# Kernel tuning notes

Measured on AMD Instinct MI355X. Metric: run time of the kernel, lower is better.

Reference implementation:

```python
import jax, jax.numpy as jnp
import numpy as np

GAMMA = 1.0

def setup_inputs() -> dict:
    key = jax.random.key(0)
    kx, ky = jax.random.split(key)
    X = jax.random.normal(kx, (8192, 64), dtype=jnp.float32)
    Y = jax.random.normal(ky, (8192, 64), dtype=jnp.float32)
    return {"X": X, "Y": Y}

def reference(X, Y):
    x2 = jnp.sum(X * X, axis=-1)            # (n,)
    y2 = jnp.sum(Y * Y, axis=-1)            # (m,)
    xy = X @ Y.T                            # (n, m)
    dist2 = x2[:, None] + y2[None, :] - 2.0 * xy
    dist2 = jnp.maximum(dist2, 0.0)         # numerical guard
    return jnp.exp(-GAMMA * dist2)
```

## Files before the change

kernel.cpp:

```cpp
#include <hip/hip_runtime.h>

typedef __attribute__((ext_vector_type(8))) short  short8_t;
typedef __attribute__((ext_vector_type(8))) unsigned short ushort8_t;
typedef __attribute__((ext_vector_type(4))) float  floatx4;

constexpr int N_ROWS = 8192;
constexpr int DIM    = 64;
constexpr int TILE   = 128;

__device__ __forceinline__ unsigned short bf16_rne(float f) {
    unsigned int u = __float_as_uint(f);
    u += 0x7FFFu + ((u >> 16) & 1u);
    return (unsigned short)(u >> 16);
}

__global__ void __launch_bounds__(256)
row_norms_kernel(const float* __restrict__ X, const float* __restrict__ Y,
                 float* __restrict__ x2, float* __restrict__ y2) {
    const int r = blockIdx.x * blockDim.x + threadIdx.x;
    const float4* xr = reinterpret_cast<const float4*>(X + (size_t)r * DIM);
    const float4* yr = reinterpret_cast<const float4*>(Y + (size_t)r * DIM);
    float sx = 0.f, sy = 0.f;
#pragma unroll
    for (int j = 0; j < DIM / 4; ++j) {
        float4 a = xr[j];
        sx = fmaf(a.x, a.x, fmaf(a.y, a.y, fmaf(a.z, a.z, fmaf(a.w, a.w, sx))));
        float4 b = yr[j];
        sy = fmaf(b.x, b.x, fmaf(b.y, b.y, fmaf(b.z, b.z, fmaf(b.w, b.w, sy))));
    }
    x2[r] = sx;
    y2[r] = sy;
}

__global__ void __launch_bounds__(256, 2)
rbf_mfma_kernel(const float* __restrict__ X, const float* __restrict__ Y,
                const float* __restrict__ x2, const float* __restrict__ y2,
                float* __restrict__ out) {
    __shared__ unsigned short smem[4 * TILE * DIM];
    constexpr int XH = 0 * TILE * DIM;
    constexpr int XL = 1 * TILE * DIM;
    constexpr int YH = 2 * TILE * DIM;
    constexpr int YL = 3 * TILE * DIM;

    const int tid  = threadIdx.x;
    const int row0 = blockIdx.y * TILE;
    const int col0 = blockIdx.x * TILE;

    {
        const int r = tid >> 1;
        const int h = tid & 1;
        const float* xr = X + (size_t)(row0 + r) * DIM + h * 32;
        const float* yr = Y + (size_t)(col0 + r) * DIM + h * 32;
        const int swz = (r & 7) * 8;
#pragma unroll
        for (int jj = 0; jj < 4; ++jj) {
            const int k0  = h * 32 + jj * 8;
            const int idx = ((r * DIM + k0) ^ swz);
            float f[8];
            *reinterpret_cast<float4*>(&f[0]) = *reinterpret_cast<const float4*>(xr + jj * 8);
            *reinterpret_cast<float4*>(&f[4]) = *reinterpret_cast<const float4*>(xr + jj * 8 + 4);
            ushort8_t hi, lo;
#pragma unroll
            for (int e = 0; e < 8; ++e) {
                unsigned short hh = bf16_rne(f[e]);
                hi[e] = hh;
                lo[e] = bf16_rne(f[e] - __uint_as_float((unsigned int)hh << 16));
            }
            *reinterpret_cast<ushort8_t*>(&smem[XH + idx]) = hi;
            *reinterpret_cast<ushort8_t*>(&smem[XL + idx]) = lo;

            *reinterpret_cast<float4*>(&f[0]) = *reinterpret_cast<const float4*>(yr + jj * 8);
            *reinterpret_cast<float4*>(&f[4]) = *reinterpret_cast<const float4*>(yr + jj * 8 + 4);
#pragma unroll
            for (int e = 0; e < 8; ++e) {
                unsigned short hh = bf16_rne(f[e]);
                hi[e] = hh;
                lo[e] = bf16_rne(f[e] - __uint_as_float((unsigned int)hh << 16));
            }
            *reinterpret_cast<ushort8_t*>(&smem[YH + idx]) = hi;
            *reinterpret_cast<ushort8_t*>(&smem[YL + idx]) = lo;
        }
    }
    __syncthreads();

    const int lane = tid & 63;
    const int w    = tid >> 6;
    const int wr   = (w >> 1) * 64;
    const int wc   = (w & 1) * 64;
    const int li   = lane & 15;
    const int lg   = lane >> 4;

    floatx4 acc[4][4] = {};

    const int kfrag = lg * 8;
#define FRAG(base, rowbase, ks)                                                \
    (*reinterpret_cast<const short8_t*>(                                       \
        &smem[(base) + ((((rowbase) + li) * DIM + (ks) * 32 + kfrag)           \
                        ^ ((((rowbase) + li) & 7) * 8))]))

    const int stepA[6] = {XH, XH, XH, XH, XL, XL};
    const int stepB[6] = {YH, YH, YL, YL, YH, YH};
    const int stepK[6] = {0, 1, 0, 1, 0, 1};
#pragma unroll
    for (int s = 0; s < 6; ++s) {
        short8_t a[4], b[4];
#pragma unroll
        for (int mi = 0; mi < 4; ++mi) a[mi] = FRAG(stepA[s], wr + mi * 16, stepK[s]);
#pragma unroll
        for (int ni = 0; ni < 4; ++ni) b[ni] = FRAG(stepB[s], wc + ni * 16, stepK[s]);
#pragma unroll
        for (int mi = 0; mi < 4; ++mi)
#pragma unroll
            for (int ni = 0; ni < 4; ++ni)
                acc[mi][ni] = __builtin_amdgcn_mfma_f32_16x16x32_bf16(
                    a[mi], b[ni], acc[mi][ni], 0, 0, 0);
    }
#undef FRAG

    float ys[4];
#pragma unroll
    for (int ni = 0; ni < 4; ++ni) ys[ni] = y2[col0 + wc + ni * 16 + li];

#pragma unroll
    for (int mi = 0; mi < 4; ++mi) {
        const int rbase = row0 + wr + mi * 16 + lg * 4;
#pragma unroll
        for (int j = 0; j < 4; ++j) {
            const float xs = x2[rbase + j];
            float* orow = out + (size_t)(rbase + j) * N_ROWS + col0 + wc + li;
#pragma unroll
            for (int ni = 0; ni < 4; ++ni) {
                float d = fmaf(-2.f, acc[mi][ni][j], xs + ys[ni]);
                d = fmaxf(d, 0.f);
                orow[ni * 16] = __expf(-d);
            }
        }
    }
}

extern "C" void kernel_launch(void* const* d_in, const int* in_sizes, int n_in,
                              void* d_out, int out_size, void* d_ws, size_t ws_size,
                              hipStream_t stream) {
    const float* X = (const float*)d_in[0];
    const float* Y = (const float*)d_in[1];
    float* out = (float*)d_out;
    float* x2  = (float*)d_ws;
    float* y2  = x2 + N_ROWS;

    row_norms_kernel<<<N_ROWS / 256, 256, 0, stream>>>(X, Y, x2, y2);

    dim3 grid(N_ROWS / TILE, N_ROWS / TILE);
    rbf_mfma_kernel<<<grid, 256, 0, stream>>>(X, Y, x2, y2, out);
}
```

Baseline: 72.68 us.

## Precompute bf16 hi/lo split panels once and DMA them into LDS

```diff
diff --git a/kernel.cpp b/kernel.cpp
--- a/kernel.cpp
+++ b/kernel.cpp
@@ -1,12 +1,13 @@
 #include <hip/hip_runtime.h>
 
-typedef __attribute__((ext_vector_type(8))) short  short8_t;
+typedef __attribute__((ext_vector_type(8))) short          short8_t;
 typedef __attribute__((ext_vector_type(8))) unsigned short ushort8_t;
-typedef __attribute__((ext_vector_type(4))) float  floatx4;
+typedef __attribute__((ext_vector_type(4))) float          floatx4;
 
 constexpr int N_ROWS = 8192;
 constexpr int DIM    = 64;
 constexpr int TILE   = 128;
+constexpr int PANEL  = TILE * DIM;
 
 __device__ __forceinline__ unsigned short bf16_rne(float f) {
     unsigned int u = __float_as_uint(f);
@@ -14,126 +15,143 @@
     return (unsigned short)(u >> 16);
 }
 
+typedef __attribute__((address_space(1))) unsigned int gu32;
+typedef __attribute__((address_space(3))) unsigned int lu32;
+__device__ __forceinline__ void gload16(const void* g, void* l) {
+    __builtin_amdgcn_global_load_lds((gu32*)g, (lu32*)l, 16, 0, 0);
+}
+
 __global__ void __launch_bounds__(256)
-row_norms_kernel(const float* __restrict__ X, const float* __restrict__ Y,
-                 float* __restrict__ x2, float* __restrict__ y2) {
-    const int r = blockIdx.x * blockDim.x + threadIdx.x;
+split_norms_kernel(const float* __restrict__ X, const float* __restrict__ Y,
+                   float* __restrict__ x2, float* __restrict__ y2,
+                   unsigned short* __restrict__ Xs, unsigned short* __restrict__ Ys) {
+    const int r  = blockIdx.x * 256 + threadIdx.x;
+    const int p  = r >> 7;
+    const int rl = r & 127;
+    const int swz = (rl & 7) * 8;
+    const size_t pb = (size_t)p * (2 * PANEL);
+
     const float4* xr = reinterpret_cast<const float4*>(X + (size_t)r * DIM);
     const float4* yr = reinterpret_cast<const float4*>(Y + (size_t)r * DIM);
+
     float sx = 0.f, sy = 0.f;
 #pragma unroll
-    for (int j = 0; j < DIM / 4; ++j) {
-        float4 a = xr[j];
-        sx = fmaf(a.x, a.x, fmaf(a.y, a.y, fmaf(a.z, a.z, fmaf(a.w, a.w, sx))));
-        float4 b = yr[j];
-        sy = fmaf(b.x, b.x, fmaf(b.y, b.y, fmaf(b.z, b.z, fmaf(b.w, b.w, sy))));
+    for (int c = 0; c < 8; ++c) {
+        const int off = (rl * DIM + c * 8) ^ swz;
+        float f[8];
+        ushort8_t hi, lo;
+
+        *reinterpret_cast<float4*>(&f[0]) = xr[2 * c];
+        *reinterpret_cast<float4*>(&f[4]) = xr[2 * c + 1];
+#pragma unroll
+        for (int e = 0; e < 8; ++e) {
+            sx = fmaf(f[e], f[e], sx);
+            unsigned short hh = bf16_rne(f[e]);
+            hi[e] = hh;
+            lo[e] = bf16_rne(f[e] - __uint_as_float((unsigned int)hh << 16));
+        }
+        *reinterpret_cast<ushort8_t*>(&Xs[pb + off])         = hi;
+        *reinterpret_cast<ushort8_t*>(&Xs[pb + PANEL + off]) = lo;
+
+        *reinterpret_cast<float4*>(&f[0]) = yr[2 * c];
+        *reinterpret_cast<float4*>(&f[4]) = yr[2 * c + 1];
+#pragma unroll
+        for (int e = 0; e < 8; ++e) {
+            sy = fmaf(f[e], f[e], sy);
+            unsigned short hh = bf16_rne(f[e]);
+            hi[e] = hh;
+            lo[e] = bf16_rne(f[e] - __uint_as_float((unsigned int)hh << 16));
+        }
+        *reinterpret_cast<ushort8_t*>(&Ys[pb + off])         = hi;
+        *reinterpret_cast<ushort8_t*>(&Ys[pb + PANEL + off]) = lo;
     }
     x2[r] = sx;
     y2[r] = sy;
 }
 
 __global__ void __launch_bounds__(256, 2)
-rbf_mfma_kernel(const float* __restrict__ X, const float* __restrict__ Y,
+rbf_mfma_kernel(const unsigned short* __restrict__ Xs,
+                const unsigned short* __restrict__ Ys,
                 const float* __restrict__ x2, const float* __restrict__ y2,
                 float* __restrict__ out) {
-    __shared__ unsigned short smem[4 * TILE * DIM];
-    constexpr int XH = 0 * TILE * DIM;
-    constexpr int XL = 1 * TILE * DIM;
-    constexpr int YH = 2 * TILE * DIM;
-    constexpr int YL = 3 * TILE * DIM;
+    __shared__ unsigned short smem[4 * PANEL];
 
     const int tid  = threadIdx.x;
+    const int lane = tid & 63;
+    const int w    = tid >> 6;
     const int row0 = blockIdx.y * TILE;
     const int col0 = blockIdx.x * TILE;
 
     {
-        const int r = tid >> 1;
-        const int h = tid & 1;
-        const float* xr = X + (size_t)(row0 + r) * DIM + h * 32;
-        const float* yr = Y + (size_t)(col0 + r) * DIM + h * 32;
-        const int swz = (r & 7) * 8;
+        const unsigned short* src =
+            (w < 2) ? Xs + (size_t)blockIdx.y * (2 * PANEL) + w * PANEL
+                    : Ys + (size_t)blockIdx.x * (2 * PANEL) + (w & 1) * PANEL;
+        unsigned short* dst = &smem[w * PANEL];
 #pragma unroll
-        for (int jj = 0; jj < 4; ++jj) {
-            const int k0  = h * 32 + jj * 8;
-            const int idx = ((r * DIM + k0) ^ swz);
-            float f[8];
-            *reinterpret_cast<float4*>(&f[0]) = *reinterpret_cast<const float4*>(xr + jj * 8);
-            *reinterpret_cast<float4*>(&f[4]) = *reinterpret_cast<const float4*>(xr + jj * 8 + 4);
-            ushort8_t hi, lo;
-#pragma unroll
-            for (int e = 0; e < 8; ++e) {
-                unsigned short hh = bf16_rne(f[e]);
-                hi[e] = hh;
-                lo[e] = bf16_rne(f[e] - __uint_as_float((unsigned int)hh << 16));
-            }
-            *reinterpret_cast<ushort8_t*>(&smem[XH + idx]) = hi;
-            *reinterpret_cast<ushort8_t*>(&smem[XL + idx]) = lo;
-
-            *reinterpret_cast<float4*>(&f[0]) = *reinterpret_cast<const float4*>(yr + jj * 8);
-            *reinterpret_cast<float4*>(&f[4]) = *reinterpret_cast<const float4*>(yr + jj * 8 + 4);
-#pragma unroll
-            for (int e = 0; e < 8; ++e) {
-                unsigned short hh = bf16_rne(f[e]);
-                hi[e] = hh;
-                lo[e] = bf16_rne(f[e] - __uint_as_float((unsigned int)hh << 16));
-            }
-            *reinterpret_cast<ushort8_t*>(&smem[YH + idx]) = hi;
-            *reinterpret_cast<ushort8_t*>(&smem[YL + idx]) = lo;
-        }
+        for (int it = 0; it < 16; ++it)
+            gload16(src + it * 512 + lane * 8, dst + it * 512);
     }
     __syncthreads();
 
-    const int lane = tid & 63;
-    const int w    = tid >> 6;
-    const int wr   = (w >> 1) * 64;
-    const int wc   = (w & 1) * 64;
-    const int li   = lane & 15;
-    const int lg   = lane >> 4;
+    const int li = lane & 15;
+    const int lg = lane >> 4;
+    const int wr = (w >> 1) * 64;
+    const int wc = (w & 1) * 64;
 
     floatx4 acc[4][4] = {};
 
-    const int kfrag = lg * 8;
-#define FRAG(base, rowbase, ks)                                                \
+#define LDF(qbase, rowbase, koff)                                              \
     (*reinterpret_cast<const short8_t*>(                                       \
-        &smem[(base) + ((((rowbase) + li) * DIM + (ks) * 32 + kfrag)           \
-                        ^ ((((rowbase) + li) & 7) * 8))]))
+        &smem[(qbase) + ((rowbase) + li) * DIM + (koff)]))
 
-    const int stepA[6] = {XH, XH, XH, XH, XL, XL};
-    const int stepB[6] = {YH, YH, YL, YL, YH, YH};
-    const int stepK[6] = {0, 1, 0, 1, 0, 1};
 #pragma unroll
-    for (int s = 0; s < 6; ++s) {
-        short8_t a[4], b[4];
+    for (int ks = 0; ks < 2; ++ks) {
+        const int koff = (ks * 32 + lg * 8) ^ ((li & 7) * 8);
+        short8_t aH[4], bH[4], aL[4], bL[4];
 #pragma unroll
-        for (int mi = 0; mi < 4; ++mi) a[mi] = FRAG(stepA[s], wr + mi * 16, stepK[s]);
+        for (int mi = 0; mi < 4; ++mi) aH[mi] = LDF(0 * PANEL, wr + mi * 16, koff);
 #pragma unroll
-        for (int ni = 0; ni < 4; ++ni) b[ni] = FRAG(stepB[s], wc + ni * 16, stepK[s]);
+        for (int ni = 0; ni < 4; ++ni) bH[ni] = LDF(2 * PANEL, wc + ni * 16, koff);
 #pragma unroll
         for (int mi = 0; mi < 4; ++mi)
 #pragma unroll
             for (int ni = 0; ni < 4; ++ni)
                 acc[mi][ni] = __builtin_amdgcn_mfma_f32_16x16x32_bf16(
-                    a[mi], b[ni], acc[mi][ni], 0, 0, 0);
+                    bH[ni], aH[mi], acc[mi][ni], 0, 0, 0);
+#pragma unroll
+        for (int ni = 0; ni < 4; ++ni) bL[ni] = LDF(3 * PANEL, wc + ni * 16, koff);
+#pragma unroll
+        for (int mi = 0; mi < 4; ++mi)
+#pragma unroll
+            for (int ni = 0; ni < 4; ++ni)
+                acc[mi][ni] = __builtin_amdgcn_mfma_f32_16x16x32_bf16(
+                    bL[ni], aH[mi], acc[mi][ni], 0, 0, 0);
+#pragma unroll
+        for (int mi = 0; mi < 4; ++mi) aL[mi] = LDF(1 * PANEL, wr + mi * 16, koff);
+#pragma unroll
+        for (int mi = 0; mi < 4; ++mi)
+#pragma unroll
+            for (int ni = 0; ni < 4; ++ni)
+                acc[mi][ni] = __builtin_amdgcn_mfma_f32_16x16x32_bf16(
+                    bH[ni], aL[mi], acc[mi][ni], 0, 0, 0);
     }
-#undef FRAG
+#undef LDF
 
-    float ys[4];
-#pragma unroll
-    for (int ni = 0; ni < 4; ++ni) ys[ni] = y2[col0 + wc + ni * 16 + li];
-
+    const int orow = row0 + wr + li;
+    const int ocol = col0 + wc + lg * 4;
 #pragma unroll
     for (int mi = 0; mi < 4; ++mi) {
-        const int rbase = row0 + wr + mi * 16 + lg * 4;
+        const float xs = x2[orow + mi * 16];
+        float* obase = out + (size_t)(orow + mi * 16) * N_ROWS + ocol;
 #pragma unroll
-        for (int j = 0; j < 4; ++j) {
-            const float xs = x2[rbase + j];
-            float* orow = out + (size_t)(rbase + j) * N_ROWS + col0 + wc + li;
-#pragma unroll
-            for (int ni = 0; ni < 4; ++ni) {
-                float d = fmaf(-2.f, acc[mi][ni][j], xs + ys[ni]);
-                d = fmaxf(d, 0.f);
-                orow[ni * 16] = __expf(-d);
-            }
+        for (int ni = 0; ni < 4; ++ni) {
+            const float4 yv = *reinterpret_cast<const float4*>(&y2[ocol + ni * 16]);
+            float4 o;
+            o.x = __expf(-fmaxf(fmaf(-2.f, acc[mi][ni][0], xs + yv.x), 0.f));
+            o.y = __expf(-fmaxf(fmaf(-2.f, acc[mi][ni][1], xs + yv.y), 0.f));
+            o.z = __expf(-fmaxf(fmaf(-2.f, acc[mi][ni][2], xs + yv.z), 0.f));
+            o.w = __expf(-fmaxf(fmaf(-2.f, acc[mi][ni][3], xs + yv.w), 0.f));
+            *reinterpret_cast<float4*>(obase + ni * 16) = o;
         }
     }
 }
@@ -144,11 +162,14 @@
     const float* X = (const float*)d_in[0];
     const float* Y = (const float*)d_in[1];
     float* out = (float*)d_out;
-    float* x2  = (float*)d_ws;
-    float* y2  = x2 + N_ROWS;
 
-    row_norms_kernel<<<N_ROWS / 256, 256, 0, stream>>>(X, Y, x2, y2);
+    float* x2 = (float*)d_ws;
+    float* y2 = x2 + N_ROWS;
+    unsigned short* Xs = (unsigned short*)(y2 + N_ROWS);
+    unsigned short* Ys = Xs + (N_ROWS / TILE) * 2 * PANEL;
+
+    split_norms_kernel<<<N_ROWS / 256, 256, 0, stream>>>(X, Y, x2, y2, Xs, Ys);
 
     dim3 grid(N_ROWS / TILE, N_ROWS / TILE);
-    rbf_mfma_kernel<<<grid, 256, 0, stream>>>(X, Y, x2, y2, out);
+    rbf_mfma_kernel<<<grid, 256, 0, stream>>>(Xs, Ys, x2, y2, out);
 }
```

After: 76.11 us. +4.7%, slower.
